# Optimization experiments

Measured on AMD Instinct MI355X. Metric: run time of the kernel, lower is better.

## Reference

```python
import jax, jax.numpy as jnp
import numpy as np

# Geometry of the single LocallyConnected2d layer being decomposed
FACTOR = 2      # number of sublayers the out_channels are split into
KH = KW = 3     # kernel size
DH = DW = 1     # stride
OH = OW = 32    # output spatial size
B, C_IN, C_OUT = 128, 32, 64
H = W = OH + KH - 1  # 34 (valid unfold with stride 1)


def setup_inputs() -> dict:
    key = jax.random.key(0)
    kx, kw_, kb = jax.random.split(key, 3)
    x = jax.random.normal(kx, (B, C_IN, H, W), dtype=jnp.float32)
    # per-location weights: (out_ch, in_ch, oh, ow, kh*kw) -- no weight sharing
    weight = jax.random.normal(kw_, (C_OUT, C_IN, OH, OW, KH * KW), dtype=jnp.float32) * 0.05
    bias = jax.random.normal(kb, (C_OUT, OH, OW), dtype=jnp.float32)
    return {"x": x, "weight": weight, "bias": bias}


def _unfold(x):
    # x: (B, C, H, W) -> patches: (B, C, OH, OW, KH*KW)
    # equivalent to torch x.unfold(2,kh,dh).unfold(3,kw,dw).reshape(..., kh*kw)
    cols = [x[:, :, i:i + DH * OH:DH, j:j + DW * OW:DW]
            for i in range(KH) for j in range(KW)]
    return jnp.stack(cols, axis=-1)


def reference(x, weight, bias):
    patches = _unfold(x)  # (B, C, OH, OW, K2)
    new_ch = weight.shape[0] // FACTOR
    outs = []
    for g in range(FACTOR):  # decomposed sublayers, concatenated on channel dim
        w_g = weight[g * new_ch:(g + 1) * new_ch]
        b_g = bias[g * new_ch:(g + 1) * new_ch]
        # out[b,o,i,j] = sum_{c,k} patches[b,c,i,j,k] * w[o,c,i,j,k] + b[o,i,j]
        o_g = jnp.einsum('bcijk,ocijk->boij', patches, w_g) + b_g[None]
        outs.append(o_g)
    return jnp.concatenate(outs, axis=1)  # (B, C_OUT, OH, OW)
```

## Files before the change

### kernel.cpp

```cpp
#include <hip/hip_runtime.h>
#include <cstdint>
#include <cstddef>

#define B_    128
#define C_    32
#define O_    64
#define H_    34
#define NPOS  1024
#define K9    9
#define BC    (B_ * C_)
#define BO    (B_ * O_)

typedef __bf16 v8bf __attribute__((ext_vector_type(8)));
typedef float  v4f  __attribute__((ext_vector_type(4)));
typedef float  f4a  __attribute__((ext_vector_type(4)));
typedef unsigned short u16x8 __attribute__((ext_vector_type(8)));

__device__ __forceinline__ unsigned short f2bf(float f) {
    union { float f; unsigned int u; } v; v.f = f;
    unsigned int u = v.u;
    return (unsigned short)((u + 0x7FFFu + ((u >> 16) & 1u)) >> 16);
}
__device__ __forceinline__ float bf2f(unsigned short s) {
    union { unsigned int u; float f; } v; v.u = ((unsigned int)s) << 16;
    return v.f;
}

__global__ __launch_bounds__(256) void repack_x(const float* __restrict__ x,
                                                unsigned short* __restrict__ x2) {
    const int bq = blockIdx.x / 17;
    const int hp = blockIdx.x % 17;
    const int b0 = bq * 2;
    const int h0 = hp * 2;
    __shared__ unsigned short tile[2][H_][66];
    const int t = threadIdx.x;

    for (int e = t; e < 2176; e += 256) {
        const int bb  = e / 1088;
        const int rem = e % 1088;
        const int c   = rem / 34;
        const int wp  = rem % 34;
        const float2 v = *(const float2*)(x +
            ((size_t)((b0 + bb) * C_ + c) * H_ + h0) * H_ + wp * 2);
        const int hh = (wp >= 17) ? 1 : 0;
        const int w  = wp * 2 - hh * 34;
        const int idx = bb * 32 + c;
        tile[hh][w][idx]     = f2bf(v.x);
        tile[hh][w + 1][idx] = f2bf(v.y);
    }
    __syncthreads();

    for (int e = t; e < 2176; e += 256) {
        const int hh  = e / 1088;
        const int rem = e % 1088;
        const int w   = rem >> 5;
        const int i2  = rem & 31;
        ushort2 pk;
        pk.x = tile[hh][w][i2 * 2];
        pk.y = tile[hh][w][i2 * 2 + 1];
        *(ushort2*)(x2 + (size_t)((h0 + hh) * H_ + w) * BC + bq * 64 + i2 * 2) = pk;
    }
}

__global__ __launch_bounds__(256, 4) void lc_fused(const unsigned short* __restrict__ x2,
                                                   const float* __restrict__ weight,
                                                   unsigned short* __restrict__ ws) {
    __shared__ __align__(16) unsigned short Wl[36 * 512];

    const int bid = blockIdx.x;
    const int jq = bid & 7;
    const int i  = (bid >> 3) & 31;
    const int oq = bid >> 8;
    const int j0 = jq * 4;
    const int o0 = oq * 16;
    const int posbase = i * 32 + j0;
    const int t = threadIdx.x;

    const float* wbase = weight + ((size_t)(o0 * C_) * NPOS + posbase) * K9;
#pragma unroll
    for (int r = 0; r < 18; ++r) {
        const int idx = r * 256 + t;
        const int pl = idx / 9;
        const int d4 = idx % 9;
        const f4a v = *(const f4a*)(wbase + (size_t)pl * (NPOS * K9) + d4 * 4);
        const int sw = ((pl >> 3) ^ (d4 & 7)) * 8 + (pl & 7);
#pragma unroll
        for (int u = 0; u < 4; ++u)
            Wl[(d4 * 4 + u) * 512 + sw] = f2bf(v[u]);
    }
    __syncthreads();

    const int wv = t >> 6;
    const int l  = t & 63;
    const int lm = l & 15;
    const int q  = l >> 4;

    v4f acc[4][2];
#pragma unroll
    for (int a = 0; a < 4; ++a)
#pragma unroll
        for (int m = 0; m < 2; ++m) acc[a][m] = (v4f){0.f, 0.f, 0.f, 0.f};

#pragma unroll
    for (int kh = 0; kh < 3; ++kh) {
        v8bf ax[6][2];
        const int rowbase = (i + kh) * H_ + j0;
#pragma unroll
        for (int w6 = 0; w6 < 6; ++w6) {
            const unsigned short* xrow = x2 + (size_t)(rowbase + w6) * BC;
            ax[w6][0] = *(const v8bf*)(xrow + (wv * 32 + lm) * C_ + q * 8);
            ax[w6][1] = *(const v8bf*)(xrow + (wv * 32 + 16 + lm) * C_ + q * 8);
        }
#pragma unroll
        for (int kw = 0; kw < 3; ++kw) {
            const int tap = kh * 3 + kw;
#pragma unroll
            for (int jj = 0; jj < 4; ++jj) {
                const int jk = jj * K9 + tap;
                const int g  = ((lm * 4 + q) ^ ((jk >> 2) & 7)) * 8;
                const v8bf bfr = *(const v8bf*)&Wl[jk * 512 + g];
                acc[jj][0] = __builtin_amdgcn_mfma_f32_16x16x32_bf16(
                    ax[kw + jj][0], bfr, acc[jj][0], 0, 0, 0);
                acc[jj][1] = __builtin_amdgcn_mfma_f32_16x16x32_bf16(
                    ax[kw + jj][1], bfr, acc[jj][1], 0, 0, 0);
            }
        }
    }

#pragma unroll
    for (int jj = 0; jj < 4; ++jj) {
        const int pos = posbase + jj;
        unsigned short* wp = ws + (size_t)pos * BO + (o0 + lm) * B_;
#pragma unroll
        for (int mt = 0; mt < 2; ++mt) {
            const int b = wv * 32 + mt * 16 + q * 4;
            ushort4 pk;
            pk.x = f2bf(acc[jj][mt][0]);
            pk.y = f2bf(acc[jj][mt][1]);
            pk.z = f2bf(acc[jj][mt][2]);
            pk.w = f2bf(acc[jj][mt][3]);
            *(ushort4*)(wp + b) = pk;
        }
    }
}

__global__ __launch_bounds__(256) void lc_fallback(const float* __restrict__ x,
                                                   const float* __restrict__ weight,
                                                   const float* __restrict__ bias,
                                                   float* __restrict__ out) {
    const int pos = blockIdx.x;
    const int i = pos >> 5, j = pos & 31;
    const int t  = threadIdx.x;
    const int wv = t >> 6;
    const int l  = t & 63;
    const int lm = l & 15;
    const int q  = l >> 4;

    float bv[4];
#pragma unroll
    for (int nt = 0; nt < 4; ++nt)
        bv[nt] = bias[(size_t)(nt * 16 + lm) * NPOS + pos];

    v4f acc[2][4];
#pragma unroll
    for (int a = 0; a < 2; ++a)
#pragma unroll
        for (int n = 0; n < 4; ++n) acc[a][n] = (v4f){0.f, 0.f, 0.f, 0.f};

    for (int k = 0; k < K9; ++k) {
        const int kh = k / 3, kw = k % 3;
        v8bf af[2], bfr[4];
#pragma unroll
        for (int mt = 0; mt < 2; ++mt) {
            const int b = wv * 32 + mt * 16 + lm;
            union { v8bf v; unsigned short s[8]; } u;
#pragma unroll
            for (int cc = 0; cc < 8; ++cc)
                u.s[cc] = f2bf(x[(((size_t)b * C_ + q * 8 + cc) * H_ + (i + kh)) * H_ + (j + kw)]);
            af[mt] = u.v;
        }
#pragma unroll
        for (int nt = 0; nt < 4; ++nt) {
            union { v8bf v; unsigned short s[8]; } u;
#pragma unroll
            for (int cc = 0; cc < 8; ++cc) {
                const int p = (nt * 16 + lm) * C_ + q * 8 + cc;
                u.s[cc] = f2bf(weight[((size_t)p * NPOS + pos) * K9 + k]);
            }
            bfr[nt] = u.v;
        }
#pragma unroll
        for (int mt = 0; mt < 2; ++mt)
#pragma unroll
            for (int nt = 0; nt < 4; ++nt)
                acc[mt][nt] = __builtin_amdgcn_mfma_f32_16x16x32_bf16(
                    af[mt], bfr[nt], acc[mt][nt], 0, 0, 0);
    }
#pragma unroll
    for (int mt = 0; mt < 2; ++mt)
#pragma unroll
        for (int nt = 0; nt < 4; ++nt) {
            const int o = nt * 16 + lm;
#pragma unroll
            for (int r = 0; r < 4; ++r) {
                const int b = wv * 32 + mt * 16 + q * 4 + r;
                out[(size_t)(b * O_ + o) * NPOS + pos] = acc[mt][nt][r] + bv[nt];
            }
        }
}

__global__ __launch_bounds__(256) void transpose_out(const unsigned short* __restrict__ ws,
                                                     const float* __restrict__ bias,
                                                     float* __restrict__ out) {
    __shared__ float tile[64][133];
    __shared__ float bsl[64];
    const int o  = blockIdx.x >> 4;
    const int pt = blockIdx.x & 15;
    const int p0 = pt * 64;
    const int t  = threadIdx.x;

    if (t < 16)
        *(float4*)&bsl[t * 4] = *(const float4*)(bias + (size_t)o * NPOS + p0 + t * 4);

#pragma unroll
    for (int it = 0; it < 4; ++it) {
        const int task = it * 256 + t;
        const int pr = task >> 4;
        const int cb = task & 15;
        const u16x8 v = *(const u16x8*)(ws + (size_t)(p0 + pr) * BO + o * B_ + cb * 8);
#pragma unroll
        for (int u = 0; u < 8; ++u)
            tile[pr][cb * 8 + u] = bf2f(v[u]);
    }
    __syncthreads();

    const int l  = t & 63;
    const int wv = t >> 6;
    const int pch = l & 7;
    const int bl  = l >> 3;
#pragma unroll
    for (int it = 0; it < 4; ++it) {
        const int b = it * 32 + wv * 8 + bl;
        float r[8];
#pragma unroll
        for (int u = 0; u < 8; ++u)
            r[u] = tile[pch * 8 + u][b] + bsl[pch * 8 + u];
        float* op = out + ((size_t)b * O_ + o) * NPOS + p0 + pch * 8;
        float4 lo = {r[0], r[1], r[2], r[3]};
        float4 hi = {r[4], r[5], r[6], r[7]};
        *(float4*)op       = lo;
        *(float4*)(op + 4) = hi;
    }
}

extern "C" void kernel_launch(void* const* d_in, const int* in_sizes, int n_in,
                              void* d_out, int out_size, void* d_ws, size_t ws_size,
                              hipStream_t stream) {
    const float* x      = (const float*)d_in[0];
    const float* weight = (const float*)d_in[1];
    const float* bias   = (const float*)d_in[2];
    float* out          = (float*)d_out;

    const size_t WSB = (size_t)NPOS * BO * sizeof(unsigned short);
    const size_t X2B = (size_t)H_ * H_ * BC * sizeof(unsigned short);

    if (ws_size >= WSB + X2B) {
        unsigned short* wsout = (unsigned short*)d_ws;
        unsigned short* x2 = (unsigned short*)((char*)d_ws + WSB);
        repack_x<<<64 * 17, 256, 0, stream>>>(x, x2);
        lc_fused<<<1024, 256, 0, stream>>>(x2, weight, wsout);
        transpose_out<<<64 * 16, 256, 0, stream>>>(wsout, bias, out);
    } else {
        lc_fallback<<<NPOS, 256, 0, stream>>>(x, weight, bias, out);
    }
}
```

Baseline: 163.2 us.

## Fuse bias and output transpose into main kernel, widen tile to 8 positions

The compute kernel now covers 8 output columns per block instead of 4, so each block can write contiguous float4 pairs straight into the final (B,O,H,W) layout with bias added. This removes the bf16 intermediate workspace and the separate transpose_out kernel, along with one launch and a full round trip of the output through memory. Weight staging is also reworked to pack four input channels per ushort4 shared-memory store. The costs are double the shared memory per block (occupancy hint lowered to 2), more accumulator registers, only 512 blocks, and 32-byte scattered output stores per lane.

```diff
diff --git a/kernel.cpp b/kernel.cpp
--- a/kernel.cpp
+++ b/kernel.cpp
@@ -14,16 +14,11 @@
 typedef __bf16 v8bf __attribute__((ext_vector_type(8)));
 typedef float  v4f  __attribute__((ext_vector_type(4)));
 typedef float  f4a  __attribute__((ext_vector_type(4)));
-typedef unsigned short u16x8 __attribute__((ext_vector_type(8)));
 
 __device__ __forceinline__ unsigned short f2bf(float f) {
     union { float f; unsigned int u; } v; v.f = f;
     unsigned int u = v.u;
     return (unsigned short)((u + 0x7FFFu + ((u >> 16) & 1u)) >> 16);
-}
-__device__ __forceinline__ float bf2f(unsigned short s) {
-    union { unsigned int u; float f; } v; v.u = ((unsigned int)s) << 16;
-    return v.f;
 }
 
 __global__ __launch_bounds__(256) void repack_x(const float* __restrict__ x,
@@ -62,31 +57,42 @@
     }
 }
 
-__global__ __launch_bounds__(256, 4) void lc_fused(const unsigned short* __restrict__ x2,
-                                                   const float* __restrict__ weight,
-                                                   unsigned short* __restrict__ ws) {
-    __shared__ __align__(16) unsigned short Wl[36 * 512];
+__global__ __launch_bounds__(256, 2) void lc_fused2(const unsigned short* __restrict__ x2,
+                                                    const float* __restrict__ weight,
+                                                    const float* __restrict__ bias,
+                                                    float* __restrict__ out) {
+    __shared__ __align__(16) unsigned short Wl[72 * 512];
 
     const int bid = blockIdx.x;
-    const int jq = bid & 7;
-    const int i  = (bid >> 3) & 31;
-    const int oq = bid >> 8;
-    const int j0 = jq * 4;
-    const int o0 = oq * 16;
+    const int lb  = (bid & 7) * 64 + (bid >> 3);
+    const int i   = lb >> 4;
+    const int jq  = (lb >> 2) & 3;
+    const int oq  = lb & 3;
+    const int j0  = jq * 8;
+    const int o0  = oq * 16;
     const int posbase = i * 32 + j0;
     const int t = threadIdx.x;
 
     const float* wbase = weight + ((size_t)(o0 * C_) * NPOS + posbase) * K9;
 #pragma unroll
-    for (int r = 0; r < 18; ++r) {
+    for (int r = 0; r < 9; ++r) {
         const int idx = r * 256 + t;
-        const int pl = idx / 9;
-        const int d4 = idx % 9;
-        const f4a v = *(const f4a*)(wbase + (size_t)pl * (NPOS * K9) + d4 * 4);
-        const int sw = ((pl >> 3) ^ (d4 & 7)) * 8 + (pl & 7);
-#pragma unroll
-        for (int u = 0; u < 4; ++u)
-            Wl[(d4 * 4 + u) * 512 + sw] = f2bf(v[u]);
+        const int plq = idx / 18;
+        const int d4  = idx % 18;
+        f4a v0 = *(const f4a*)(wbase + (size_t)(plq * 4 + 0) * (NPOS * K9) + d4 * 4);
+        f4a v1 = *(const f4a*)(wbase + (size_t)(plq * 4 + 1) * (NPOS * K9) + d4 * 4);
+        f4a v2 = *(const f4a*)(wbase + (size_t)(plq * 4 + 2) * (NPOS * K9) + d4 * 4);
+        f4a v3 = *(const f4a*)(wbase + (size_t)(plq * 4 + 3) * (NPOS * K9) + d4 * 4);
+        const int colbase = (((plq >> 1) ^ (d4 & 7)) * 8) + (plq & 1) * 4;
+#pragma unroll
+        for (int u = 0; u < 4; ++u) {
+            ushort4 pk;
+            pk.x = f2bf(v0[u]);
+            pk.y = f2bf(v1[u]);
+            pk.z = f2bf(v2[u]);
+            pk.w = f2bf(v3[u]);
+            *(ushort4*)&Wl[(d4 * 4 + u) * 512 + colbase] = pk;
+        }
     }
     __syncthreads();
 
@@ -95,18 +101,18 @@
     const int lm = l & 15;
     const int q  = l >> 4;
 
-    v4f acc[4][2];
-#pragma unroll
-    for (int a = 0; a < 4; ++a)
+    v4f acc[8][2];
+#pragma unroll
+    for (int a = 0; a < 8; ++a)
 #pragma unroll
         for (int m = 0; m < 2; ++m) acc[a][m] = (v4f){0.f, 0.f, 0.f, 0.f};
 
 #pragma unroll
     for (int kh = 0; kh < 3; ++kh) {
-        v8bf ax[6][2];
+        v8bf ax[10][2];
         const int rowbase = (i + kh) * H_ + j0;
 #pragma unroll
-        for (int w6 = 0; w6 < 6; ++w6) {
+        for (int w6 = 0; w6 < 10; ++w6) {
             const unsigned short* xrow = x2 + (size_t)(rowbase + w6) * BC;
             ax[w6][0] = *(const v8bf*)(xrow + (wv * 32 + lm) * C_ + q * 8);
             ax[w6][1] = *(const v8bf*)(xrow + (wv * 32 + 16 + lm) * C_ + q * 8);
@@ -115,7 +121,7 @@
         for (int kw = 0; kw < 3; ++kw) {
             const int tap = kh * 3 + kw;
 #pragma unroll
-            for (int jj = 0; jj < 4; ++jj) {
+            for (int jj = 0; jj < 8; ++jj) {
                 const int jk = jj * K9 + tap;
                 const int g  = ((lm * 4 + q) ^ ((jk >> 2) & 7)) * 8;
                 const v8bf bfr = *(const v8bf*)&Wl[jk * 512 + g];
@@ -127,19 +133,21 @@
         }
     }
 
-#pragma unroll
-    for (int jj = 0; jj < 4; ++jj) {
-        const int pos = posbase + jj;
-        unsigned short* wp = ws + (size_t)pos * BO + (o0 + lm) * B_;
-#pragma unroll
-        for (int mt = 0; mt < 2; ++mt) {
-            const int b = wv * 32 + mt * 16 + q * 4;
-            ushort4 pk;
-            pk.x = f2bf(acc[jj][mt][0]);
-            pk.y = f2bf(acc[jj][mt][1]);
-            pk.z = f2bf(acc[jj][mt][2]);
-            pk.w = f2bf(acc[jj][mt][3]);
-            *(ushort4*)(wp + b) = pk;
+    const float* bp = bias + (size_t)(o0 + lm) * NPOS + posbase;
+    const f4a bv0 = *(const f4a*)bp;
+    const f4a bv1 = *(const f4a*)(bp + 4);
+#pragma unroll
+    for (int mt = 0; mt < 2; ++mt) {
+#pragma unroll
+        for (int r2 = 0; r2 < 4; ++r2) {
+            const int b = wv * 32 + mt * 16 + q * 4 + r2;
+            float* op = out + ((size_t)b * O_ + (o0 + lm)) * NPOS + posbase;
+            f4a lo = {acc[0][mt][r2] + bv0[0], acc[1][mt][r2] + bv0[1],
+                      acc[2][mt][r2] + bv0[2], acc[3][mt][r2] + bv0[3]};
+            f4a hi = {acc[4][mt][r2] + bv1[0], acc[5][mt][r2] + bv1[1],
+                      acc[6][mt][r2] + bv1[2], acc[7][mt][r2] + bv1[3]};
+            *(f4a*)op       = lo;
+            *(f4a*)(op + 4) = hi;
         }
     }
 }
@@ -209,50 +217,6 @@
         }
 }
 
-__global__ __launch_bounds__(256) void transpose_out(const unsigned short* __restrict__ ws,
-                                                     const float* __restrict__ bias,
-                                                     float* __restrict__ out) {
-    __shared__ float tile[64][133];
-    __shared__ float bsl[64];
-    const int o  = blockIdx.x >> 4;
-    const int pt = blockIdx.x & 15;
-    const int p0 = pt * 64;
-    const int t  = threadIdx.x;
-
-    if (t < 16)
-        *(float4*)&bsl[t * 4] = *(const float4*)(bias + (size_t)o * NPOS + p0 + t * 4);
-
-#pragma unroll
-    for (int it = 0; it < 4; ++it) {
-        const int task = it * 256 + t;
-        const int pr = task >> 4;
-        const int cb = task & 15;
-        const u16x8 v = *(const u16x8*)(ws + (size_t)(p0 + pr) * BO + o * B_ + cb * 8);
-#pragma unroll
-        for (int u = 0; u < 8; ++u)
-            tile[pr][cb * 8 + u] = bf2f(v[u]);
-    }
-    __syncthreads();
-
-    const int l  = t & 63;
-    const int wv = t >> 6;
-    const int pch = l & 7;
-    const int bl  = l >> 3;
-#pragma unroll
-    for (int it = 0; it < 4; ++it) {
-        const int b = it * 32 + wv * 8 + bl;
-        float r[8];
-#pragma unroll
-        for (int u = 0; u < 8; ++u)
-            r[u] = tile[pch * 8 + u][b] + bsl[pch * 8 + u];
-        float* op = out + ((size_t)b * O_ + o) * NPOS + p0 + pch * 8;
-        float4 lo = {r[0], r[1], r[2], r[3]};
-        float4 hi = {r[4], r[5], r[6], r[7]};
-        *(float4*)op       = lo;
-        *(float4*)(op + 4) = hi;
-    }
-}
-
 extern "C" void kernel_launch(void* const* d_in, const int* in_sizes, int n_in,
                               void* d_out, int out_size, void* d_ws, size_t ws_size,
                               hipStream_t stream) {
@@ -261,15 +225,12 @@
     const float* bias   = (const float*)d_in[2];
     float* out          = (float*)d_out;
 
-    const size_t WSB = (size_t)NPOS * BO * sizeof(unsigned short);
     const size_t X2B = (size_t)H_ * H_ * BC * sizeof(unsigned short);
 
-    if (ws_size >= WSB + X2B) {
-        unsigned short* wsout = (unsigned short*)d_ws;
-        unsigned short* x2 = (unsigned short*)((char*)d_ws + WSB);
+    if (ws_size >= X2B) {
+        unsigned short* x2 = (unsigned short*)d_ws;
         repack_x<<<64 * 17, 256, 0, stream>>>(x, x2);
-        lc_fused<<<1024, 256, 0, stream>>>(x2, weight, wsout);
-        transpose_out<<<64 * 16, 256, 0, stream>>>(wsout, bias, out);
+        lc_fused2<<<512, 256, 0, stream>>>(x2, weight, bias, out);
     } else {
         lc_fallback<<<NPOS, 256, 0, stream>>>(x, weight, bias, out);
     }
```

After: 156.7 us. 1.04x faster.
